# Performance work log

Measured on AMD Instinct MI355X. Metric: run time of the kernel, lower is better.

Reference implementation:

```python
import jax, jax.numpy as jnp
import numpy as np
from jax import lax

B, CIN, L = 2, 768, 1024
DM, DI, DS, DTR, DC = 512, 1024, 16, 32, 4  # d_model, d_inner, d_state, dt_rank, d_conv


def _conv1d(x, w, b, pad, groups=1):
    # x: (B, Cin, L), w: (Cout, Cin//groups, K)
    y = lax.conv_general_dilated(x, w, (1,), [pad], dimension_numbers=('NCH', 'OIH', 'NCH'),
                                 feature_group_count=groups)
    return y + b[None, :, None]


def _gnorm(x, g, b, groups=32, eps=1e-5):
    Bx, C, Lx = x.shape
    xg = x.reshape(Bx, groups, C // groups, Lx)
    m = xg.mean((2, 3), keepdims=True)
    v = xg.var((2, 3), keepdims=True)
    xg = (xg - m) * lax.rsqrt(v + eps)
    return xg.reshape(Bx, C, Lx) * g[None, :, None] + b[None, :, None]


def _selective_scan(u, delta, A, Bm, Cm, D):
    # u, delta: (B, L, DI); Bm, Cm: (B, L, DS); A: (DI, DS); D: (DI,)
    def step(h, inp):
        d, b, c, x = inp  # d,x: (B,DI); b,c: (B,DS)
        h = jnp.exp(d[..., None] * A) * h + (d * x)[..., None] * b[:, None, :]
        y = jnp.einsum('bds,bs->bd', h, c)
        return h, y
    h0 = jnp.zeros((u.shape[0], A.shape[0], A.shape[1]), u.dtype)
    xs = tuple(jnp.moveaxis(t, 1, 0) for t in (delta, Bm, Cm, u))
    _, ys = lax.scan(step, h0, xs)
    return jnp.moveaxis(ys, 0, 1) + u * D


def _mamba_dir(xz, cv_w, cv_b, xp_w, dt_w, dt_b, Alog, D):
    x, z = jnp.split(xz, 2, axis=1)                       # each (B, DI, L)
    x = _conv1d(x, cv_w, cv_b, (DC - 1, 0), groups=DI)    # causal depthwise conv
    x = jax.nn.silu(x)
    xT = x.transpose(0, 2, 1)                             # (B, L, DI)
    x_dbl = xT @ xp_w.T                                   # (B, L, DTR+2*DS)
    dt, Bm, Cm = jnp.split(x_dbl, [DTR, DTR + DS], axis=-1)
    delta = jax.nn.softplus(dt @ dt_w.T + dt_b)           # (B, L, DI)
    y = _selective_scan(xT, delta, -jnp.exp(Alog), Bm, Cm, D)
    return y * jax.nn.silu(z.transpose(0, 2, 1))


def _forward(x, conv1_w, conv1_b, gn1_g, gn1_b, conv2_w, conv2_b, gn2_g, gn2_b,
             conv3_w, conv3_b, gn3_g, gn3_b, ln_g, ln_b, in_proj_w, out_proj_w,
             cv_w_f, cv_b_f, xp_w_f, dt_w_f, dt_b_f, Alog_f, D_f,
             cv_w_r, cv_b_r, xp_w_r, dt_w_r, dt_b_r, Alog_r, D_r):
    # CNN stem: (Conv1d k3 p1 -> GroupNorm(32) -> ReLU) x 3, 768->128->256->512
    h = jax.nn.relu(_gnorm(_conv1d(x, conv1_w, conv1_b, (1, 1)), gn1_g, gn1_b))
    h = jax.nn.relu(_gnorm(_conv1d(h, conv2_w, conv2_b, (1, 1)), gn2_g, gn2_b))
    h = jax.nn.relu(_gnorm(_conv1d(h, conv3_w, conv3_b, (1, 1)), gn3_g, gn3_b))  # (B,512,L)
    res = h
    # MaskMambaBlock: LayerNorm -> bidirectional ViM -> residual; mask is all-ones (no-op)
    t = h.transpose(0, 2, 1)                               # (B, L, DM)
    mu = t.mean(-1, keepdims=True)
    var = t.var(-1, keepdims=True)
    t = (t - mu) * lax.rsqrt(var + 1e-5) * ln_g + ln_b
    xz = (t @ in_proj_w.T).transpose(0, 2, 1)              # (B, 2*DI, L) shared for both dirs
    yf = _mamba_dir(xz, cv_w_f, cv_b_f, xp_w_f, dt_w_f, dt_b_f, Alog_f, D_f)
    yr = _mamba_dir(jnp.flip(xz, -1), cv_w_r, cv_b_r, xp_w_r, dt_w_r, dt_b_r, Alog_r, D_r)
    y = yf + jnp.flip(yr, 1)                               # (B, L, DI)
    out = (y @ out_proj_w.T).transpose(0, 2, 1)            # (B, DM, L)
    return res + out


def setup_inputs() -> dict:
    key = jax.random.key(0)
    ks = iter(jax.random.split(key, 64))
    p = lambda shape, s=0.02: jax.random.normal(next(ks), shape, jnp.float32) * s
    d = {"x": jax.random.normal(next(ks), (B, CIN, L), jnp.float32)}
    for i, (ci, co) in enumerate([(CIN, 128), (128, 256), (256, 512)], 1):
        d[f"conv{i}_w"] = p((co, ci, 3))
        d[f"conv{i}_b"] = jnp.zeros((co,))
        d[f"gn{i}_g"] = jnp.ones((co,))
        d[f"gn{i}_b"] = jnp.zeros((co,))
    d["ln_g"] = jnp.ones((DM,))
    d["ln_b"] = jnp.zeros((DM,))
    d["in_proj_w"] = p((2 * DI, DM))
    d["out_proj_w"] = p((DM, DI))
    for s in ("f", "r"):
        d[f"cv_w_{s}"] = p((DI, 1, DC), 0.1)
        d[f"cv_b_{s}"] = jnp.zeros((DI,))
        d[f"xp_w_{s}"] = p((DTR + 2 * DS, DI))
        d[f"dt_w_{s}"] = p((DI, DTR), 0.1)
        d[f"dt_b_{s}"] = p((DI,), 0.5) - 4.0  # softplus(dt) small, like Mamba dt init
        d[f"Alog_{s}"] = jnp.log(jnp.tile(jnp.arange(1, DS + 1, dtype=jnp.float32)[None, :], (DI, 1)))
        d[f"D_{s}"] = jnp.ones((DI,))
    return d


def reference(x, conv1_w, conv1_b, gn1_g, gn1_b, conv2_w, conv2_b, gn2_g, gn2_b,
              conv3_w, conv3_b, gn3_g, gn3_b, ln_g, ln_b, in_proj_w, out_proj_w,
              cv_w_f, cv_b_f, xp_w_f, dt_w_f, dt_b_f, Alog_f, D_f,
              cv_w_r, cv_b_r, xp_w_r, dt_w_r, dt_b_r, Alog_r, D_r):
    return _forward(x, conv1_w, conv1_b, gn1_g, gn1_b, conv2_w, conv2_b, gn2_g, gn2_b,
                    conv3_w, conv3_b, gn3_g, gn3_b, ln_g, ln_b, in_proj_w, out_proj_w,
                    cv_w_f, cv_b_f, xp_w_f, dt_w_f, dt_b_f, Alog_f, D_f,
                    cv_w_r, cv_b_r, xp_w_r, dt_w_r, dt_b_r, Alog_r, D_r)
```

## Files before the change

### kernel.cpp

```cpp
#include <hip/hip_runtime.h>
#include <hip/hip_bf16.h>
#include <math.h>

#define LL 1024
#define NC 16
#define CS 64

typedef __attribute__((ext_vector_type(8))) short short8_t;
typedef __attribute__((ext_vector_type(4))) float f32x4;

__device__ __forceinline__ float sigmoidf_(float x){ return 1.f/(1.f+__expf(-x)); }
__device__ __forceinline__ unsigned short f2bu(float x){
  unsigned int u = __float_as_uint(x);
  unsigned int r = (u + 0x7fffu + ((u>>16)&1u)) >> 16;
  return (unsigned short)r;
}
__device__ __forceinline__ float bu2f(unsigned short u){
  return __uint_as_float(((unsigned int)u)<<16);
}
__device__ __forceinline__ void gl2lds16(const void* g, void* l){
  __builtin_amdgcn_global_load_lds(
      (const __attribute__((address_space(1))) unsigned int*)g,
      (__attribute__((address_space(3))) unsigned int*)l, 16, 0, 0);
}

__global__ __launch_bounds__(256) void gn_relu_k(
    float* __restrict__ io, const float* __restrict__ g, const float* __restrict__ bt,
    int C, int Cg)
{
  int b = blockIdx.x >> 5;
  int grp = blockIdx.x & 31;
  int n = Cg * LL;
  float* p = io + ((size_t)b*C + (size_t)grp*Cg)*LL;
  int tid = threadIdx.x;
  float s=0.f, s2=0.f;
  for (int i=tid; i<n; i+=256){ float v=p[i]; s+=v; s2+=v*v; }
  __shared__ float red[10];
  #pragma unroll
  for (int off=32; off; off>>=1){ s+=__shfl_down(s,off); s2+=__shfl_down(s2,off); }
  if ((tid&63)==0){ red[tid>>6]=s; red[4+(tid>>6)]=s2; }
  __syncthreads();
  if (tid==0){
    float S=red[0]+red[1]+red[2]+red[3];
    float S2=red[4]+red[5]+red[6]+red[7];
    float mean = S/(float)n;
    float var = S2/(float)n - mean*mean;
    red[8]=mean; red[9]=rsqrtf(var+1e-5f);
  }
  __syncthreads();
  float mean=red[8], rstd=red[9];
  const float* gp = g + grp*Cg;
  const float* bp = bt + grp*Cg;
  for (int i=tid; i<n; i+=256){
    int co = i >> 10;
    float v = (p[i]-mean)*rstd*gp[co] + bp[co];
    p[i] = fmaxf(v, 0.f);
  }
}

__global__ __launch_bounds__(64) void ln_k(
    const float* __restrict__ h, const float* __restrict__ g, const float* __restrict__ bt,
    float* __restrict__ tout)
{
  int bl = blockIdx.x;
  int b = bl >> 10, l = bl & 1023;
  int lane = threadIdx.x;
  const float* base = h + (size_t)b*512*LL + l;
  float v[8]; float s=0.f, s2=0.f;
  #pragma unroll
  for (int j=0;j<8;++j){ v[j] = base[(size_t)(lane + j*64)*LL]; s+=v[j]; s2+=v[j]*v[j]; }
  #pragma unroll
  for (int off=32; off; off>>=1){ s+=__shfl_xor(s,off); s2+=__shfl_xor(s2,off); }
  float mean = s*(1.f/512.f);
  float rstd = rsqrtf(s2*(1.f/512.f) - mean*mean + 1e-5f);
  float* o = tout + (size_t)bl*512;
  #pragma unroll
  for (int j=0;j<8;++j){ int c = lane + j*64; o[c] = (v[j]-mean)*rstd*g[c] + bt[c]; }
}

template<int MODE>
__global__ __launch_bounds__(256) void reduceK_k(
    const float* __restrict__ P, const float* __restrict__ bias,
    const float* __restrict__ res, float* __restrict__ out,
    int M, int N, int KS, unsigned short* __restrict__ d16)
{
  int i = blockIdx.x*256 + threadIdx.x;
  if (i >= N*M) return;
  float s = 0.f;
  for (int k=0;k<KS;++k) s += P[(size_t)k*((size_t)N*M) + i];
  if (MODE==0){ out[i] = s; return; }
  if (MODE==3){
    out[i] = s;
    int c = i & 63;
    if (c < 32) d16[(size_t)(i>>6)*32 + c] = f2bu(s);
    return;
  }
  int n = i / M, m = i - n*M;
  int b = n >> 10, l = n & 1023;
  size_t o = ((size_t)b*M + m)*LL + l;
  if (MODE==1) out[o] = s + bias[m];
  else         out[o] = s + res[o];
}

__global__ __launch_bounds__(256) void ts_split3_k(
    const float* __restrict__ src, unsigned short* __restrict__ dst, int Cin)
{
  __shared__ float sx[32][35];
  int b = blockIdx.z;
  int l0 = blockIdx.x*32, ci0 = blockIdx.y*32;
  int tid = threadIdx.x;
  const float* sb = src + ((size_t)b*Cin + ci0)*LL;
  for (int idx = tid; idx < 32*34; idx += 256){
    int r = idx / 34, c = idx - r*34;
    int lp = l0 - 1 + c;
    sx[r][c] = (lp >= 0 && lp < LL) ? sb[(size_t)r*LL + lp] : 0.f;
  }
  __syncthreads();
  int K = 3*Cin, K3 = 9*Cin;
  int lr = tid >> 5, cl = tid & 31;
  #pragma unroll
  for (int p=0;p<4;++p){
    int l = lr + p*8;
    unsigned short* drow = dst + (size_t)(b*LL + l0 + l)*K3;
    #pragma unroll
    for (int tap=0; tap<3; ++tap){
      float v = sx[cl][l + tap];
      unsigned short hi = f2bu(v);
      unsigned short lo = f2bu(v - bu2f(hi));
      int kk = tap*Cin + ci0 + cl;
      drow[kk] = hi; drow[K + kk] = hi; drow[2*K + kk] = lo;
    }
  }
}

__global__ __launch_bounds__(256) void wsplit3_conv_k(
    const float* __restrict__ w, unsigned short* __restrict__ dst, int Cout, int Cin)
{
  int i = blockIdx.x*256 + threadIdx.x;
  if (i >= Cout*Cin) return;
  int co = i / Cin, ci = i - co*Cin;
  int K = 3*Cin, K3 = 9*Cin;
  unsigned short* drow = dst + (size_t)co*K3;
  #pragma unroll
  for (int tap=0; tap<3; ++tap){
    float v = w[(size_t)(co*Cin + ci)*3 + tap];
    unsigned short hi = f2bu(v);
    unsigned short lo = f2bu(v - bu2f(hi));
    int kk = tap*Cin + ci;
    drow[kk] = hi; drow[K + kk] = lo; drow[2*K + kk] = hi;
  }
}

template<int PAT>
__global__ __launch_bounds__(256) void split3_k(
    const float* __restrict__ src, unsigned short* __restrict__ dst,
    int R, int K, int ld)
{
  int i = blockIdx.x*256 + threadIdx.x;
  int kq = K >> 2;
  if (i >= R*kq) return;
  int r = i / kq, k4 = (i - r*kq)*4;
  float4 v = *(const float4*)&src[(size_t)r*ld + k4];
  float vv[4] = {v.x, v.y, v.z, v.w};
  unsigned short hi[4], lo[4];
  #pragma unroll
  for (int j=0;j<4;++j){ hi[j]=f2bu(vv[j]); lo[j]=f2bu(vv[j]-bu2f(hi[j])); }
  unsigned short* d0 = dst + (size_t)r*3*K + k4;
  ushort4 h4 = make_ushort4(hi[0],hi[1],hi[2],hi[3]);
  ushort4 l4 = make_ushort4(lo[0],lo[1],lo[2],lo[3]);
  *(ushort4*)d0 = h4;
  *(ushort4*)(d0 + K)   = (PAT==0) ? l4 : h4;
  *(ushort4*)(d0 + 2*K) = (PAT==0) ? h4 : l4;
}

__global__ __launch_bounds__(256) void split1_k(
    const float* __restrict__ src, unsigned short* __restrict__ dst,
    int R, int K, int ld, int k0)
{
  int i = blockIdx.x*256 + threadIdx.x;
  int kq = K >> 2;
  if (i >= R*kq) return;
  int r = i / kq, k4 = (i - r*kq)*4;
  float4 v = *(const float4*)&src[(size_t)r*ld + k0 + k4];
  *(ushort4*)(dst + (size_t)r*K + k4) =
      make_ushort4(f2bu(v.x), f2bu(v.y), f2bu(v.z), f2bu(v.w));
}

__global__ __launch_bounds__(256) void gated_split_k(
    const float* __restrict__ y0, const float* __restrict__ y1,
    const float* __restrict__ xz, unsigned short* __restrict__ dst)
{
  __shared__ float sz[32][33];
  int b = blockIdx.z;
  int l0 = blockIdx.x*32, d0 = blockIdx.y*32;
  int tid = threadIdx.x;
  const float* zb = xz + ((size_t)b*2048 + 1024 + d0)*LL + l0;
  for (int idx = tid; idx < 1024; idx += 256){
    int r = idx >> 5, c = idx & 31;
    sz[r][c] = zb[(size_t)r*LL + c];
  }
  __syncthreads();
  int lr = tid >> 5, dd = tid & 31;
  #pragma unroll
  for (int p=0;p<4;++p){
    int l = lr + p*8;
    size_t n = (size_t)b*LL + l0 + l;
    float zv = sz[dd][l];
    float y = y0[n*1024 + d0 + dd] + y1[n*1024 + d0 + dd];
    dst[n*1024 + d0 + dd] = f2bu(y * (zv * sigmoidf_(zv)));
  }
}

template<int BM, int BK, int EPI>
__global__ __launch_bounds__(256) void gemm_bf3(
    const unsigned short* __restrict__ A, const unsigned short* __restrict__ B,
    const float* __restrict__ bias, void* __restrict__ Cv,
    int M, int N, int K3)
{
  constexpr int BN = 64;
  constexpr int RB = 2*BK;
  constexpr int RPL = 1024/RB;
  constexpr int ALD = BM/RPL;
  constexpr int BLD = BN/RPL;
  constexpr int NL = ALD + BLD;
  constexpr int FM = BM/32;
  constexpr int KH = BK/32;
  __shared__ __align__(16) char smem[(BM+BN)*RB];
  char* As = smem;
  char* Bs = smem + BM*RB;
  int tid = threadIdx.x;
  int w = tid >> 6, lane = tid & 63;
  int wm = w & 1, wn = w >> 1;
  int n0 = blockIdx.x*BN, m0 = blockIdx.y*BM;
  int kper = K3 / gridDim.z;
  int kbeg = blockIdx.z * kper;

  int lr, sc;
  if (BK == 64){ lr = lane>>3; sc = (lane&7) ^ lr; }
  else         { lr = lane>>2; sc = (lane&3) ^ ((lr>>1)&3); }
  size_t lsrc = (size_t)lr*K3 + sc*8;

  f32x4 acc[FM][2];
  #pragma unroll
  for (int i=0;i<FM;++i){ acc[i][0] = (f32x4){0,0,0,0}; acc[i][1] = (f32x4){0,0,0,0}; }

  int r16 = lane & 15, g4 = lane >> 4;
  for (int k = kbeg; k < kbeg + kper; k += BK){
    for (int j = w; j < NL; j += 4){
      if (j < ALD){
        gl2lds16(A + (size_t)(m0 + j*RPL)*K3 + k + lsrc, As + j*(RPL*RB));
      } else {
        int jb = j - ALD;
        gl2lds16(B + (size_t)(n0 + jb*RPL)*K3 + k + lsrc, Bs + jb*(RPL*RB));
      }
    }
    __syncthreads();
    #pragma unroll
    for (int kh=0; kh<KH; ++kh){
      int c = kh*4 + g4;
      int rb0 = wn*32 + r16, rb1 = rb0 + 16;
      int pb0 = (BK==64) ? (c ^ (rb0&7)) : (c ^ ((rb0>>1)&3));
      int pb1 = (BK==64) ? (c ^ (rb1&7)) : (c ^ ((rb1>>1)&3));
      short8_t bf0 = *(short8_t*)&Bs[rb0*RB + pb0*16];
      short8_t bf1 = *(short8_t*)&Bs[rb1*RB + pb1*16];
      #pragma unroll
      for (int i2=0;i2<FM;++i2){
        int ra = wm*(BM/2) + i2*16 + r16;
        int pa = (BK==64) ? (c ^ (ra&7)) : (c ^ ((ra>>1)&3));
        short8_t af = *(short8_t*)&As[ra*RB + pa*16];
        acc[i2][0] = __builtin_amdgcn_mfma_f32_16x16x32_bf16(af, bf0, acc[i2][0], 0,0,0);
        acc[i2][1] = __builtin_amdgcn_mfma_f32_16x16x32_bf16(af, bf1, acc[i2][1], 0,0,0);
      }
    }
    __syncthreads();
  }
  #pragma unroll
  for (int i2=0;i2<FM;++i2){
    #pragma unroll
    for (int j=0;j<2;++j){
      #pragma unroll
      for (int r=0;r<4;++r){
        int m = m0 + wm*(BM/2) + i2*16 + (g4*4 + r);
        int n = n0 + wn*32 + j*16 + r16;
        float v = acc[i2][j][r];
        if (EPI==0){
          ((float*)Cv)[(size_t)blockIdx.z*((size_t)N*M) + (size_t)n*M + m] = v;
        } else if (EPI==1){
          int b = n>>10, l = n&1023;
          ((float*)Cv)[((size_t)b*M + m)*LL + l] = v;
        } else {
          float xv = v + bias[m];
          float sp = (xv > 20.f) ? xv : log1pf(__expf(xv));
          ((unsigned short*)Cv)[(size_t)n*M + m] = f2bu(sp);
        }
      }
    }
  }
}

__global__ __launch_bounds__(256) void dwconv_k(
    const float* __restrict__ xz, const float* __restrict__ cw,
    const float* __restrict__ cb, unsigned short* __restrict__ outT, int rev)
{
  __shared__ float sx[64][73];
  int l0 = blockIdx.x * 64;
  int d0 = blockIdx.y * 64;
  int b = blockIdx.z;
  int tid = threadIdx.x;
  const float* base = xz + ((size_t)b*2048 + d0)*LL;
  for (int idx = tid; idx < 64*67; idx += 256) {
    int r = idx / 67, i = idx - r*67;
    int lp = l0 - 3 + i;
    float v = 0.f;
    if (lp >= 0) v = base[(size_t)r*LL + (rev ? (LL-1-lp) : lp)];
    sx[r][i] = v;
  }
  __syncthreads();
  int dof = tid & 63;
  int lq = tid >> 6;
  int d = d0 + dof;
  float4 w4 = *(const float4*)(cw + (size_t)d*4);
  float bv = cb[d];
  unsigned short* orow = outT + (size_t)b*LL*1024 + d;
  #pragma unroll
  for (int j=0;j<16;++j){
    int lr = lq + j*4;
    float acc = bv + w4.x*sx[dof][lr] + w4.y*sx[dof][lr+1]
                   + w4.z*sx[dof][lr+2] + w4.w*sx[dof][lr+3];
    orow[(size_t)(l0+lr)*1024] = f2bu(acc * sigmoidf_(acc));
  }
}

__global__ __launch_bounds__(256) void scan1_k(
    const unsigned short* __restrict__ de0, const unsigned short* __restrict__ de1,
    const unsigned short* __restrict__ u0, const unsigned short* __restrict__ u1,
    const float* __restrict__ xd0, const float* __restrict__ xd1,
    const float* __restrict__ al0, const float* __restrict__ al1,
    float* __restrict__ Pbuf, float* __restrict__ Sbuf)
{
  __shared__ float sBC[CS][32];
  int zc = blockIdx.z, dir = zc>>1, b = zc&1;
  const unsigned short* de = dir? de1:de0;
  const unsigned short* uT = dir? u1:u0;
  const float* xd = dir? xd1:xd0;
  const float* al = dir? al1:al0;
  int t = threadIdx.x;
  int d = blockIdx.x*128 + (t>>1);
  int sh = (t&1)*8;
  int l0 = blockIdx.y*CS;
  size_t nrow = (size_t)b*1024 + l0;
  for (int idx = t; idx < CS*32; idx += 256){
    int r = idx >> 5, c = idx & 31;
    sBC[r][c] = xd[(nrow + r)*64 + 32 + c];
  }
  __syncthreads();
  float A[8], h[8], P[8];
  #pragma unroll
  for (int j=0;j<8;++j){ A[j] = -expf(al[d*16 + sh + j]); h[j]=0.f; P[j]=1.f; }
  const unsigned short* dep = de + nrow*1024 + d;
  const unsigned short* up  = uT + nrow*1024 + d;
  for (int l=0; l<CS; ++l){
    float dv = bu2f(dep[(size_t)l*1024]);
    float uv = bu2f(up[(size_t)l*1024]);
    float du = dv*uv;
    #pragma unroll
    for (int j=0;j<8;++j){
      float a = __expf(dv*A[j]);
      h[j] = a*h[j] + du*sBC[l][sh+j];
      P[j] *= a;
    }
  }
  size_t sb = (size_t)blockIdx.y*65536 + (size_t)(zc*1024 + d)*16 + sh;
  *(float4*)&Pbuf[sb]   = make_float4(P[0],P[1],P[2],P[3]);
  *(float4*)&Pbuf[sb+4] = make_float4(P[4],P[5],P[6],P[7]);
  *(float4*)&Sbuf[sb]   = make_float4(h[0],h[1],h[2],h[3]);
  *(float4*)&Sbuf[sb+4] = make_float4(h[4],h[5],h[6],h[7]);
}

__global__ __launch_bounds__(256) void scan2_k(
    const float* __restrict__ Pbuf, const float* __restrict__ Sbuf,
    float* __restrict__ Hbuf)
{
  int seq = blockIdx.x*256 + threadIdx.x;
  float H = 0.f;
  #pragma unroll
  for (int cch=0; cch<NC; ++cch){
    Hbuf[(size_t)cch*65536 + seq] = H;
    H = Pbuf[(size_t)cch*65536 + seq]*H + Sbuf[(size_t)cch*65536 + seq];
  }
}

__global__ __launch_bounds__(256) void scan3_k(
    const unsigned short* __restrict__ de0, const unsigned short* __restrict__ de1,
    const unsigned short* __restrict__ u0, const unsigned short* __restrict__ u1,
    const float* __restrict__ xd0, const float* __restrict__ xd1,
    const float* __restrict__ al0, const float* __restrict__ al1,
    const float* __restrict__ dd0, const float* __restrict__ dd1,
    const float* __restrict__ Hbuf,
    float* __restrict__ y0, float* __restrict__ y1)
{
  __shared__ float sBC[CS][32];
  int zc = blockIdx.z, dir = zc>>1, b = zc&1;
  const unsigned short* de = dir? de1:de0;
  const unsigned short* uT = dir? u1:u0;
  const float* xd = dir? xd1:xd0;
  const float* al = dir? al1:al0;
  const float* DD = dir? dd1:dd0;
  float* y = dir? y1:y0;
  int t = threadIdx.x;
  int d = blockIdx.x*128 + (t>>1);
  int sh = (t&1)*8;
  int l0 = blockIdx.y*CS;
  size_t nrow = (size_t)b*1024 + l0;
  for (int idx = t; idx < CS*32; idx += 256){
    int r = idx >> 5, c = idx & 31;
    sBC[r][c] = xd[(nrow + r)*64 + 32 + c];
  }
  __syncthreads();
  float A[8], h[8];
  size_t sb = (size_t)blockIdx.y*65536 + (size_t)(zc*1024 + d)*16 + sh;
  float4 h03 = *(const float4*)&Hbuf[sb];
  float4 h47 = *(const float4*)&Hbuf[sb+4];
  h[0]=h03.x; h[1]=h03.y; h[2]=h03.z; h[3]=h03.w;
  h[4]=h47.x; h[5]=h47.y; h[6]=h47.z; h[7]=h47.w;
  #pragma unroll
  for (int j=0;j<8;++j) A[j] = -expf(al[d*16 + sh + j]);
  float Dd = DD[d];
  const unsigned short* dep = de + nrow*1024 + d;
  const unsigned short* up  = uT + nrow*1024 + d;
  float* yb = y + (size_t)b*LL*1024 + d;
  for (int l=0; l<CS; ++l){
    float dv = bu2f(dep[(size_t)l*1024]);
    float uv = bu2f(up[(size_t)l*1024]);
    float du = dv*uv;
    float pa = 0.f;
    #pragma unroll
    for (int j=0;j<8;++j){
      float a = __expf(dv*A[j]);
      h[j] = a*h[j] + du*sBC[l][sh+j];
      pa += h[j]*sBC[l][16+sh+j];
    }
    pa += __shfl_xor(pa, 1);
    if ((t&1)==0){
      int lo = dir ? (1023 - l0 - l) : (l0 + l);
      yb[(size_t)lo*1024] = pa + uv*Dd;
    }
  }
}

extern "C" void kernel_launch(void* const* d_in, const int* in_sizes, int n_in,
                              void* d_out, int out_size, void* d_ws, size_t ws_size,
                              hipStream_t stream)
{
  const float* x   = (const float*)d_in[0];
  const float* c1w = (const float*)d_in[1];  const float* c1b = (const float*)d_in[2];
  const float* g1g = (const float*)d_in[3];  const float* g1b = (const float*)d_in[4];
  const float* c2w = (const float*)d_in[5];  const float* c2b = (const float*)d_in[6];
  const float* g2g = (const float*)d_in[7];  const float* g2b = (const float*)d_in[8];
  const float* c3w = (const float*)d_in[9];  const float* c3b = (const float*)d_in[10];
  const float* g3g = (const float*)d_in[11]; const float* g3b = (const float*)d_in[12];
  const float* lng = (const float*)d_in[13]; const float* lnb = (const float*)d_in[14];
  const float* ipw = (const float*)d_in[15]; const float* opw = (const float*)d_in[16];
  const float* cvw[2]  = {(const float*)d_in[17], (const float*)d_in[24]};
  const float* cvb[2]  = {(const float*)d_in[18], (const float*)d_in[25]};
  const float* xpw[2]  = {(const float*)d_in[19], (const float*)d_in[26]};
  const float* dtw[2]  = {(const float*)d_in[20], (const float*)d_in[27]};
  const float* dtb[2]  = {(const float*)d_in[21], (const float*)d_in[28]};
  const float* alog[2] = {(const float*)d_in[22], (const float*)d_in[29]};
  const float* Dp[2]   = {(const float*)d_in[23], (const float*)d_in[30]};

  float* ws = (float*)d_ws;
  float* h3  = ws;
  float* h1  = ws + 1048576;
  float* h2  = ws + 1310720;
  float* t   = ws + 1835008;
  float* xzb = ws + 2883584;
  unsigned short* Wb = (unsigned short*)(ws + 7077888);
  unsigned short* Bsb = (unsigned short*)(ws + 8650752);
  float* yy0 = ws + 11796480;
  float* yy1 = ws + 13893632;
  float* PART = ws + 15990784;
  unsigned short* xcv[2] = { (unsigned short*)(ws + 18087936),
                             (unsigned short*)(ws + 18087936) + 2097152 };
  float* xdb[2] = { ws + 1048576, ws + 1179648 };
  unsigned short* dl[2] = { (unsigned short*)PART, (unsigned short*)PART + 2097152 };
  float* Pb = ws + 2883584;
  float* Sb = ws + 4980736;
  float* Hb = ws + 1835008;
  float* pxp = ws + 8650752;
  unsigned short* dtB = (unsigned short*)(ws + 9175040);
  float* out = (float*)d_out;

  ts_split3_k<<<dim3(32,24,2), 256, 0, stream>>>(x, Bsb, 768);
  wsplit3_conv_k<<<384, 256, 0, stream>>>(c1w, Wb, 128, 768);
  gemm_bf3<64,64,0><<<dim3(32,2,4), 256, 0, stream>>>(Wb, Bsb, nullptr, PART, 128, 2048, 6912);
  reduceK_k<1><<<1024, 256, 0, stream>>>(PART, c1b, nullptr, h1, 128, 2048, 4, nullptr);
  gn_relu_k<<<64, 256, 0, stream>>>(h1, g1g, g1b, 128, 4);

  ts_split3_k<<<dim3(32,4,2), 256, 0, stream>>>(h1, Bsb, 128);
  wsplit3_conv_k<<<128, 256, 0, stream>>>(c2w, Wb, 256, 128);
  gemm_bf3<64,64,0><<<dim3(32,4,2), 256, 0, stream>>>(Wb, Bsb, nullptr, PART, 256, 2048, 1152);
  reduceK_k<1><<<2048, 256, 0, stream>>>(PART, c2b, nullptr, h2, 256, 2048, 2, nullptr);
  gn_relu_k<<<64, 256, 0, stream>>>(h2, g2g, g2b, 256, 8);

  ts_split3_k<<<dim3(32,8,2), 256, 0, stream>>>(h2, Bsb, 256);
  wsplit3_conv_k<<<512, 256, 0, stream>>>(c3w, Wb, 512, 256);
  gemm_bf3<128,64,0><<<dim3(32,4,2), 256, 0, stream>>>(Wb, Bsb, nullptr, PART, 512, 2048, 2304);
  reduceK_k<1><<<4096, 256, 0, stream>>>(PART, c3b, nullptr, h3, 512, 2048, 2, nullptr);
  gn_relu_k<<<64, 256, 0, stream>>>(h3, g3g, g3b, 512, 16);

  ln_k<<<2048, 64, 0, stream>>>(h3, lng, lnb, t);
  split3_k<0><<<1024, 256, 0, stream>>>(ipw, Wb, 2048, 512, 512);
  split3_k<1><<<1024, 256, 0, stream>>>(t, Bsb, 2048, 512, 512);
  gemm_bf3<128,64,1><<<dim3(32,16,1), 256, 0, stream>>>(Wb, Bsb, nullptr, xzb, 2048, 2048, 1536);

  dwconv_k<<<dim3(16,16,2), 256, 0, stream>>>(xzb, cvw[0], cvb[0], xcv[0], 0);
  dwconv_k<<<dim3(16,16,2), 256, 0, stream>>>(xzb, cvw[1], cvb[1], xcv[1], 1);
  for (int s2=0; s2<2; ++s2){
    split1_k<<<64, 256, 0, stream>>>(xpw[s2], Wb, 64, 1024, 1024, 0);
    gemm_bf3<64,64,0><<<dim3(32,1,4), 256, 0, stream>>>(Wb, xcv[s2], nullptr, pxp, 64, 2048, 1024);
    reduceK_k<3><<<512, 256, 0, stream>>>(pxp, nullptr, nullptr, xdb[s2], 64, 2048, 4, dtB);
    split1_k<<<32, 256, 0, stream>>>(dtw[s2], Wb, 1024, 32, 32, 0);
    gemm_bf3<128,32,2><<<dim3(32,8,1), 256, 0, stream>>>(Wb, dtB, dtb[s2], dl[s2], 1024, 2048, 32);
  }

  scan1_k<<<dim3(8,NC,4), 256, 0, stream>>>(
      dl[0], dl[1], xcv[0], xcv[1], xdb[0], xdb[1], alog[0], alog[1], Pb, Sb);
  scan2_k<<<256, 256, 0, stream>>>(Pb, Sb, Hb);
  scan3_k<<<dim3(8,NC,4), 256, 0, stream>>>(
      dl[0], dl[1], xcv[0], xcv[1], xdb[0], xdb[1], alog[0], alog[1],
      Dp[0], Dp[1], Hb, yy0, yy1);

  gated_split_k<<<dim3(32,32,2), 256, 0, stream>>>(yy0, yy1, xzb, Bsb);
  split1_k<<<512, 256, 0, stream>>>(opw, Wb, 512, 1024, 1024, 0);
  gemm_bf3<128,64,0><<<dim3(32,4,2), 256, 0, stream>>>(Wb, Bsb, nullptr, PART, 512, 2048, 1024);
  reduceK_k<2><<<4096, 256, 0, stream>>>(PART, nullptr, h3, out, 512, 2048, 2, nullptr);
}
```

Baseline: 492.5 us.

## Fuse LayerNorm with bf16 split, batch both scan directions, widen in_proj GEMM tile

LayerNorm now writes the hi/hi/lo bf16 split operand directly, so the fp32 temporary and a separate split kernel are gone. The depthwise conv, x_proj GEMM, its reduction and the dt_proj GEMM now handle both scan directions in a single launch each, using a DUAL mode in the GEMM template. The in_proj GEMM uses a 128x128 tile instead of 128x64, giving more reuse per block but fewer blocks and more accumulator registers. Launch count and intermediate memory traffic drop, in exchange for more complex indexing and possible occupancy loss in the larger GEMM.

```diff
diff --git a/kernel.cpp b/kernel.cpp
--- a/kernel.cpp
+++ b/kernel.cpp
@@ -58,9 +58,9 @@
   }
 }
 
-__global__ __launch_bounds__(64) void ln_k(
+__global__ __launch_bounds__(64) void ln_split_k(
     const float* __restrict__ h, const float* __restrict__ g, const float* __restrict__ bt,
-    float* __restrict__ tout)
+    unsigned short* __restrict__ dst)
 {
   int bl = blockIdx.x;
   int b = bl >> 10, l = bl & 1023;
@@ -68,38 +68,55 @@
   const float* base = h + (size_t)b*512*LL + l;
   float v[8]; float s=0.f, s2=0.f;
   #pragma unroll
-  for (int j=0;j<8;++j){ v[j] = base[(size_t)(lane + j*64)*LL]; s+=v[j]; s2+=v[j]*v[j]; }
+  for (int j=0;j<8;++j){ v[j] = base[(size_t)(lane*8 + j)*LL]; s+=v[j]; s2+=v[j]*v[j]; }
   #pragma unroll
   for (int off=32; off; off>>=1){ s+=__shfl_xor(s,off); s2+=__shfl_xor(s2,off); }
   float mean = s*(1.f/512.f);
   float rstd = rsqrtf(s2*(1.f/512.f) - mean*mean + 1e-5f);
-  float* o = tout + (size_t)bl*512;
-  #pragma unroll
-  for (int j=0;j<8;++j){ int c = lane + j*64; o[c] = (v[j]-mean)*rstd*g[c] + bt[c]; }
+  unsigned short hi[8], lo[8];
+  #pragma unroll
+  for (int j=0;j<8;++j){
+    int c = lane*8 + j;
+    float f = (v[j]-mean)*rstd*g[c] + bt[c];
+    hi[j] = f2bu(f); lo[j] = f2bu(f - bu2f(hi[j]));
+  }
+  unsigned short* row = dst + (size_t)bl*1536 + lane*8;
+  *(ushort4*)&row[0] = make_ushort4(hi[0],hi[1],hi[2],hi[3]);
+  *(ushort4*)&row[4] = make_ushort4(hi[4],hi[5],hi[6],hi[7]);
+  *(ushort4*)&row[512] = make_ushort4(hi[0],hi[1],hi[2],hi[3]);
+  *(ushort4*)&row[516] = make_ushort4(hi[4],hi[5],hi[6],hi[7]);
+  *(ushort4*)&row[1024] = make_ushort4(lo[0],lo[1],lo[2],lo[3]);
+  *(ushort4*)&row[1028] = make_ushort4(lo[4],lo[5],lo[6],lo[7]);
 }
 
 template<int MODE>
 __global__ __launch_bounds__(256) void reduceK_k(
     const float* __restrict__ P, const float* __restrict__ bias,
     const float* __restrict__ res, float* __restrict__ out,
-    int M, int N, int KS, unsigned short* __restrict__ d16)
+    int M, int N, int KS)
 {
   int i = blockIdx.x*256 + threadIdx.x;
   if (i >= N*M) return;
   float s = 0.f;
   for (int k=0;k<KS;++k) s += P[(size_t)k*((size_t)N*M) + i];
-  if (MODE==0){ out[i] = s; return; }
-  if (MODE==3){
-    out[i] = s;
-    int c = i & 63;
-    if (c < 32) d16[(size_t)(i>>6)*32 + c] = f2bu(s);
-    return;
-  }
   int n = i / M, m = i - n*M;
   int b = n >> 10, l = n & 1023;
   size_t o = ((size_t)b*M + m)*LL + l;
   if (MODE==1) out[o] = s + bias[m];
   else         out[o] = s + res[o];
+}
+
+__global__ __launch_bounds__(256) void reducexp_k(
+    const float* __restrict__ P, float* __restrict__ out, unsigned short* __restrict__ d16)
+{
+  int i = blockIdx.x*256 + threadIdx.x;
+  int dir = i >> 17, ii = i & 131071;
+  float s = 0.f;
+  #pragma unroll
+  for (int k=0;k<4;++k) s += P[(size_t)(dir*4 + k)*131072 + ii];
+  out[i] = s;
+  int c = ii & 63;
+  if (c < 32) d16[(size_t)(i>>6)*32 + c] = f2bu(s);
 }
 
 __global__ __launch_bounds__(256) void ts_split3_k(
@@ -151,7 +168,6 @@
   }
 }
 
-template<int PAT>
 __global__ __launch_bounds__(256) void split3_k(
     const float* __restrict__ src, unsigned short* __restrict__ dst,
     int R, int K, int ld)
@@ -169,8 +185,8 @@
   ushort4 h4 = make_ushort4(hi[0],hi[1],hi[2],hi[3]);
   ushort4 l4 = make_ushort4(lo[0],lo[1],lo[2],lo[3]);
   *(ushort4*)d0 = h4;
-  *(ushort4*)(d0 + K)   = (PAT==0) ? l4 : h4;
-  *(ushort4*)(d0 + 2*K) = (PAT==0) ? h4 : l4;
+  *(ushort4*)(d0 + K)   = l4;
+  *(ushort4*)(d0 + 2*K) = h4;
 }
 
 __global__ __launch_bounds__(256) void split1_k(
@@ -183,6 +199,21 @@
   int r = i / kq, k4 = (i - r*kq)*4;
   float4 v = *(const float4*)&src[(size_t)r*ld + k0 + k4];
   *(ushort4*)(dst + (size_t)r*K + k4) =
+      make_ushort4(f2bu(v.x), f2bu(v.y), f2bu(v.z), f2bu(v.w));
+}
+
+__global__ __launch_bounds__(256) void split1x2_k(
+    const float* __restrict__ s0, const float* __restrict__ s1,
+    unsigned short* __restrict__ d, int R, int K, int dstr)
+{
+  int i = blockIdx.x*256 + threadIdx.x;
+  int kq = K >> 2, tot = R*kq;
+  if (i >= 2*tot) return;
+  int dir = i >= tot, ii = i - dir*tot;
+  const float* src = dir ? s1 : s0;
+  int r = ii / kq, k4 = (ii - r*kq)*4;
+  float4 v = *(const float4*)&src[(size_t)r*K + k4];
+  *(ushort4*)(d + (size_t)dir*dstr + (size_t)r*K + k4) =
       make_ushort4(f2bu(v.x), f2bu(v.y), f2bu(v.z), f2bu(v.w));
 }
 
@@ -211,38 +242,52 @@
   }
 }
 
-template<int BM, int BK, int EPI>
+template<int BM, int BN, int BK, int EPI, int DUAL>
 __global__ __launch_bounds__(256) void gemm_bf3(
     const unsigned short* __restrict__ A, const unsigned short* __restrict__ B,
-    const float* __restrict__ bias, void* __restrict__ Cv,
-    int M, int N, int K3)
-{
-  constexpr int BN = 64;
+    const float* __restrict__ bias, const float* __restrict__ bias2,
+    void* __restrict__ Cv, int M, int N, int K3,
+    int AStr, int BStr, long CStr)
+{
   constexpr int RB = 2*BK;
   constexpr int RPL = 1024/RB;
   constexpr int ALD = BM/RPL;
   constexpr int BLD = BN/RPL;
   constexpr int NL = ALD + BLD;
   constexpr int FM = BM/32;
+  constexpr int WCOL = BN/2;
+  constexpr int FN = WCOL/16;
   constexpr int KH = BK/32;
   __shared__ __align__(16) char smem[(BM+BN)*RB];
   char* As = smem;
   char* Bs = smem + BM*RB;
   int tid = threadIdx.x;
   int w = tid >> 6, lane = tid & 63;
-  int wm = w & 1, wn = w >> 1;
+  int wm, wn;
+  if (BN == 128){ wm = w>>1; wn = w&1; }
+  else          { wm = w&1;  wn = w>>1; }
   int n0 = blockIdx.x*BN, m0 = blockIdx.y*BM;
-  int kper = K3 / gridDim.z;
-  int kbeg = blockIdx.z * kper;
+
+  int zz = blockIdx.z, nz = gridDim.z, dir = 0;
+  if (DUAL){
+    int hz = nz >> 1;
+    dir = zz / hz; zz -= dir*hz; nz = hz;
+    A += (size_t)dir*AStr; B += (size_t)dir*BStr;
+    if (dir && bias2) bias = bias2;
+  }
+  int kper = K3 / nz;
+  int kbeg = zz * kper;
 
   int lr, sc;
   if (BK == 64){ lr = lane>>3; sc = (lane&7) ^ lr; }
   else         { lr = lane>>2; sc = (lane&3) ^ ((lr>>1)&3); }
   size_t lsrc = (size_t)lr*K3 + sc*8;
 
-  f32x4 acc[FM][2];
-  #pragma unroll
-  for (int i=0;i<FM;++i){ acc[i][0] = (f32x4){0,0,0,0}; acc[i][1] = (f32x4){0,0,0,0}; }
+  f32x4 acc[FM][FN];
+  #pragma unroll
+  for (int i=0;i<FM;++i)
+    #pragma unroll
+    for (int j=0;j<FN;++j) acc[i][j] = (f32x4){0,0,0,0};
 
   int r16 = lane & 15, g4 = lane >> 4;
   for (int k = kbeg; k < kbeg + kper; k += BK){
@@ -258,18 +303,21 @@
     #pragma unroll
     for (int kh=0; kh<KH; ++kh){
       int c = kh*4 + g4;
-      int rb0 = wn*32 + r16, rb1 = rb0 + 16;
-      int pb0 = (BK==64) ? (c ^ (rb0&7)) : (c ^ ((rb0>>1)&3));
-      int pb1 = (BK==64) ? (c ^ (rb1&7)) : (c ^ ((rb1>>1)&3));
-      short8_t bf0 = *(short8_t*)&Bs[rb0*RB + pb0*16];
-      short8_t bf1 = *(short8_t*)&Bs[rb1*RB + pb1*16];
+      short8_t bf[FN];
+      #pragma unroll
+      for (int j2=0;j2<FN;++j2){
+        int rb = wn*WCOL + j2*16 + r16;
+        int pb = (BK==64) ? (c ^ (rb&7)) : (c ^ ((rb>>1)&3));
+        bf[j2] = *(short8_t*)&Bs[rb*RB + pb*16];
+      }
       #pragma unroll
       for (int i2=0;i2<FM;++i2){
         int ra = wm*(BM/2) + i2*16 + r16;
         int pa = (BK==64) ? (c ^ (ra&7)) : (c ^ ((ra>>1)&3));
         short8_t af = *(short8_t*)&As[ra*RB + pa*16];
-        acc[i2][0] = __builtin_amdgcn_mfma_f32_16x16x32_bf16(af, bf0, acc[i2][0], 0,0,0);
-        acc[i2][1] = __builtin_amdgcn_mfma_f32_16x16x32_bf16(af, bf1, acc[i2][1], 0,0,0);
+        #pragma unroll
+        for (int j2=0;j2<FN;++j2)
+          acc[i2][j2] = __builtin_amdgcn_mfma_f32_16x16x32_bf16(af, bf[j2], acc[i2][j2], 0,0,0);
       }
     }
     __syncthreads();
@@ -277,12 +325,12 @@
   #pragma unroll
   for (int i2=0;i2<FM;++i2){
     #pragma unroll
-    for (int j=0;j<2;++j){
+    for (int j2=0;j2<FN;++j2){
       #pragma unroll
       for (int r=0;r<4;++r){
         int m = m0 + wm*(BM/2) + i2*16 + (g4*4 + r);
-        int n = n0 + wn*32 + j*16 + r16;
-        float v = acc[i2][j][r];
+        int n = n0 + wn*WCOL + j2*16 + r16;
+        float v = acc[i2][j2][r];
         if (EPI==0){
           ((float*)Cv)[(size_t)blockIdx.z*((size_t)N*M) + (size_t)n*M + m] = v;
         } else if (EPI==1){
@@ -291,7 +339,7 @@
         } else {
           float xv = v + bias[m];
           float sp = (xv > 20.f) ? xv : log1pf(__expf(xv));
-          ((unsigned short*)Cv)[(size_t)n*M + m] = f2bu(sp);
+          (((unsigned short*)Cv) + (size_t)dir*CStr)[(size_t)n*M + m] = f2bu(sp);
         }
       }
     }
@@ -299,13 +347,18 @@
 }
 
 __global__ __launch_bounds__(256) void dwconv_k(
-    const float* __restrict__ xz, const float* __restrict__ cw,
-    const float* __restrict__ cb, unsigned short* __restrict__ outT, int rev)
+    const float* __restrict__ xz, const float* __restrict__ cw0,
+    const float* __restrict__ cb0, const float* __restrict__ cw1,
+    const float* __restrict__ cb1, unsigned short* __restrict__ outT0)
 {
   __shared__ float sx[64][73];
+  int zc = blockIdx.z;
+  int b = zc & 1, rev = zc >> 1;
+  const float* cw = rev ? cw1 : cw0;
+  const float* cb = rev ? cb1 : cb0;
+  unsigned short* outT = outT0 + (size_t)rev*2097152;
   int l0 = blockIdx.x * 64;
   int d0 = blockIdx.y * 64;
-  int b = blockIdx.z;
   int tid = threadIdx.x;
   const float* base = xz + ((size_t)b*2048 + d0)*LL;
   for (int idx = tid; idx < 64*67; idx += 256) {
@@ -473,7 +526,7 @@
   float* h3  = ws;
   float* h1  = ws + 1048576;
   float* h2  = ws + 1310720;
-  float* t   = ws + 1835008;
+  float* Hb  = ws + 1835008;
   float* xzb = ws + 2883584;
   unsigned short* Wb = (unsigned short*)(ws + 7077888);
   unsigned short* Bsb = (unsigned short*)(ws + 8650752);
@@ -486,43 +539,46 @@
   unsigned short* dl[2] = { (unsigned short*)PART, (unsigned short*)PART + 2097152 };
   float* Pb = ws + 2883584;
   float* Sb = ws + 4980736;
-  float* Hb = ws + 1835008;
   float* pxp = ws + 8650752;
-  unsigned short* dtB = (unsigned short*)(ws + 9175040);
+  unsigned short* dtB = (unsigned short*)(ws + 9699328);
+  unsigned short* WbXp = Wb;
+  unsigned short* WbDt = Wb + 131072;
   float* out = (float*)d_out;
 
   ts_split3_k<<<dim3(32,24,2), 256, 0, stream>>>(x, Bsb, 768);
   wsplit3_conv_k<<<384, 256, 0, stream>>>(c1w, Wb, 128, 768);
-  gemm_bf3<64,64,0><<<dim3(32,2,4), 256, 0, stream>>>(Wb, Bsb, nullptr, PART, 128, 2048, 6912);
-  reduceK_k<1><<<1024, 256, 0, stream>>>(PART, c1b, nullptr, h1, 128, 2048, 4, nullptr);
+  gemm_bf3<64,64,64,0,0><<<dim3(32,2,4), 256, 0, stream>>>(
+      Wb, Bsb, nullptr, nullptr, PART, 128, 2048, 6912, 0,0,0);
+  reduceK_k<1><<<1024, 256, 0, stream>>>(PART, c1b, nullptr, h1, 128, 2048, 4);
   gn_relu_k<<<64, 256, 0, stream>>>(h1, g1g, g1b, 128, 4);
 
   ts_split3_k<<<dim3(32,4,2), 256, 0, stream>>>(h1, Bsb, 128);
   wsplit3_conv_k<<<128, 256, 0, stream>>>(c2w, Wb, 256, 128);
-  gemm_bf3<64,64,0><<<dim3(32,4,2), 256, 0, stream>>>(Wb, Bsb, nullptr, PART, 256, 2048, 1152);
-  reduceK_k<1><<<2048, 256, 0, stream>>>(PART, c2b, nullptr, h2, 256, 2048, 2, nullptr);
+  gemm_bf3<64,64,64,0,0><<<dim3(32,4,2), 256, 0, stream>>>(
+      Wb, Bsb, nullptr, nullptr, PART, 256, 2048, 1152, 0,0,0);
+  reduceK_k<1><<<2048, 256, 0, stream>>>(PART, c2b, nullptr, h2, 256, 2048, 2);
   gn_relu_k<<<64, 256, 0, stream>>>(h2, g2g, g2b, 256, 8);
 
   ts_split3_k<<<dim3(32,8,2), 256, 0, stream>>>(h2, Bsb, 256);
   wsplit3_conv_k<<<512, 256, 0, stream>>>(c3w, Wb, 512, 256);
-  gemm_bf3<128,64,0><<<dim3(32,4,2), 256, 0, stream>>>(Wb, Bsb, nullptr, PART, 512, 2048, 2304);
-  reduceK_k<1><<<4096, 256, 0, stream>>>(PART, c3b, nullptr, h3, 512, 2048, 2, nullptr);
+  gemm_bf3<128,64,64,0,0><<<dim3(32,4,2), 256, 0, stream>>>(
+      Wb, Bsb, nullptr, nullptr, PART, 512, 2048, 2304, 0,0,0);
+  reduceK_k<1><<<4096, 256, 0, stream>>>(PART, c3b, nullptr, h3, 512, 2048, 2);
   gn_relu_k<<<64, 256, 0, stream>>>(h3, g3g, g3b, 512, 16);
 
-  ln_k<<<2048, 64, 0, stream>>>(h3, lng, lnb, t);
-  split3_k<0><<<1024, 256, 0, stream>>>(ipw, Wb, 2048, 512, 512);
-  split3_k<1><<<1024, 256, 0, stream>>>(t, Bsb, 2048, 512, 512);
-  gemm_bf3<128,64,1><<<dim3(32,16,1), 256, 0, stream>>>(Wb, Bsb, nullptr, xzb, 2048, 2048, 1536);
-
-  dwconv_k<<<dim3(16,16,2), 256, 0, stream>>>(xzb, cvw[0], cvb[0], xcv[0], 0);
-  dwconv_k<<<dim3(16,16,2), 256, 0, stream>>>(xzb, cvw[1], cvb[1], xcv[1], 1);
-  for (int s2=0; s2<2; ++s2){
-    split1_k<<<64, 256, 0, stream>>>(xpw[s2], Wb, 64, 1024, 1024, 0);
-    gemm_bf3<64,64,0><<<dim3(32,1,4), 256, 0, stream>>>(Wb, xcv[s2], nullptr, pxp, 64, 2048, 1024);
-    reduceK_k<3><<<512, 256, 0, stream>>>(pxp, nullptr, nullptr, xdb[s2], 64, 2048, 4, dtB);
-    split1_k<<<32, 256, 0, stream>>>(dtw[s2], Wb, 1024, 32, 32, 0);
-    gemm_bf3<128,32,2><<<dim3(32,8,1), 256, 0, stream>>>(Wb, dtB, dtb[s2], dl[s2], 1024, 2048, 32);
-  }
+  ln_split_k<<<2048, 64, 0, stream>>>(h3, lng, lnb, Bsb);
+  split3_k<<<1024, 256, 0, stream>>>(ipw, Wb, 2048, 512, 512);
+  gemm_bf3<128,128,64,1,0><<<dim3(16,16,1), 256, 0, stream>>>(
+      Wb, Bsb, nullptr, nullptr, xzb, 2048, 2048, 1536, 0,0,0);
+
+  dwconv_k<<<dim3(16,16,4), 256, 0, stream>>>(xzb, cvw[0], cvb[0], cvw[1], cvb[1], xcv[0]);
+  split1x2_k<<<128, 256, 0, stream>>>(xpw[0], xpw[1], WbXp, 64, 1024, 65536);
+  gemm_bf3<64,64,64,0,1><<<dim3(32,1,8), 256, 0, stream>>>(
+      WbXp, xcv[0], nullptr, nullptr, pxp, 64, 2048, 1024, 65536, 2097152, 0);
+  reducexp_k<<<1024, 256, 0, stream>>>(pxp, xdb[0], dtB);
+  split1x2_k<<<64, 256, 0, stream>>>(dtw[0], dtw[1], WbDt, 1024, 32, 32768);
+  gemm_bf3<128,64,32,2,1><<<dim3(32,8,2), 256, 0, stream>>>(
+      WbDt, dtB, dtb[0], dtb[1], dl[0], 1024, 2048, 32, 32768, 65536, 2097152);
 
   scan1_k<<<dim3(8,NC,4), 256, 0, stream>>>(
       dl[0], dl[1], xcv[0], xcv[1], xdb[0], xdb[1], alog[0], alog[1], Pb, Sb);
@@ -533,6 +589,7 @@
 
   gated_split_k<<<dim3(32,32,2), 256, 0, stream>>>(yy0, yy1, xzb, Bsb);
   split1_k<<<512, 256, 0, stream>>>(opw, Wb, 512, 1024, 1024, 0);
-  gemm_bf3<128,64,0><<<dim3(32,4,2), 256, 0, stream>>>(Wb, Bsb, nullptr, PART, 512, 2048, 1024);
-  reduceK_k<2><<<4096, 256, 0, stream>>>(PART, nullptr, h3, out, 512, 2048, 2, nullptr);
-}
+  gemm_bf3<128,64,64,0,0><<<dim3(32,4,2), 256, 0, stream>>>(
+      Wb, Bsb, nullptr, nullptr, PART, 512, 2048, 1024, 0,0,0);
+  reduceK_k<2><<<4096, 256, 0, stream>>>(PART, nullptr, h3, out, 512, 2048, 2);
+}
```

Result: faster. 460.7 us (-6.5%).
